# Performance work log

Measured on AMD Instinct MI355X. Metric: run time of the kernel, lower is better.

## Reference

```python
import jax, jax.numpy as jnp
import numpy as np

B, L, DIM, H = 2, 2048, 2048, 16
D = DIM // H
EPS = 1e-6
CAP = 50.0
SCALE = D ** -0.5


def _rms_norm(x, w):
    # x: [B,H,L,D], normalize over last dim
    scale = jax.lax.rsqrt(jnp.maximum(jnp.mean(x * x, axis=-1, keepdims=True), EPS))
    return w * x * scale


def _rotate_half(x):
    x1, x2 = jnp.split(x, 2, axis=-1)
    return jnp.concatenate([-x2, x1], axis=-1)


def setup_inputs() -> dict:
    key = jax.random.key(0)
    ks = jax.random.split(key, 6)
    x = jax.random.normal(ks[0], (B, L, DIM), dtype=jnp.float32)
    w_qkv = jax.random.normal(ks[1], (3 * DIM, DIM), dtype=jnp.float32) * (DIM ** -0.5)
    w_out = jax.random.normal(ks[2], (DIM, DIM), dtype=jnp.float32) * (DIM ** -0.5)
    q_norm_w = jnp.ones((D,), dtype=jnp.float32)
    k_norm_w = jnp.ones((D,), dtype=jnp.float32)
    # rope tables [L, D]
    inv_freq = 1.0 / (10000.0 ** (np.arange(0, D, 2, dtype=np.float32) / D))
    t = np.arange(L, dtype=np.float32)
    freqs = np.outer(t, inv_freq)  # [L, D/2]
    emb = np.concatenate([freqs, freqs], axis=-1)  # [L, D]
    cos = jnp.asarray(np.cos(emb), dtype=jnp.float32)
    sin = jnp.asarray(np.sin(emb), dtype=jnp.float32)
    # additive causal mask [1,1,L,L]
    causal = np.triu(np.full((L, L), -1e9, dtype=np.float32), k=1)
    mask = jnp.asarray(causal)[None, None]
    return {"x": x, "w_qkv": w_qkv, "w_out": w_out, "q_norm_w": q_norm_w,
            "k_norm_w": k_norm_w, "cos": cos, "sin": sin, "mask": mask}


def reference(x, w_qkv, w_out, q_norm_w, k_norm_w, cos, sin, mask):
    b, l, _ = x.shape
    qkv = jnp.einsum('bld,ed->ble', x, w_qkv).reshape(b, l, 3, H, D)
    q, k, v = [jnp.transpose(qkv[:, :, i], (0, 2, 1, 3)) for i in range(3)]  # [B,H,L,D]
    q = _rms_norm(q, q_norm_w)
    k = _rms_norm(k, k_norm_w)
    # rope: cos/sin are [L,D] -> [1,1,L,D]
    c = cos[-l:, :][None, None]
    s = sin[-l:, :][None, None]
    q = q * c + _rotate_half(q) * s
    k = k * c + _rotate_half(k) * s
    attn = jnp.einsum('bhqd,bhkd->bhqk', q, k) * SCALE
    attn = jnp.tanh(attn / CAP) * CAP + mask
    probs = jax.nn.softmax(attn, axis=-1)
    o = jnp.einsum('bhqk,bhkd->bhqd', probs, v)
    o = jnp.transpose(o, (0, 2, 1, 3)).reshape(b, l, H * D)
    out = jnp.einsum('bld,ed->ble', o, w_out)
    return (out, (k, v))
```

## Files before the change

### kernel.cpp

```cpp
#include <hip/hip_runtime.h>
#include <hip/hip_bf16.h>
#include <stdint.h>

#define LL 2048
#define DD 128
#define HH 16

typedef float f32x4 __attribute__((ext_vector_type(4)));
typedef float f32x2 __attribute__((ext_vector_type(2)));
typedef short bf16x8 __attribute__((ext_vector_type(8)));
typedef short short4v __attribute__((ext_vector_type(4)));
typedef float float4v __attribute__((ext_vector_type(4)));

__device__ __forceinline__ float bf2f(short s) {
  union { unsigned u; float f; } v; v.u = ((unsigned)(unsigned short)s) << 16; return v.f;
}
__device__ __forceinline__ short f2bf(float f) {
  union { float f; unsigned u; } v; v.f = f;
  unsigned u = v.u;
  u += 0x7fffu + ((u >> 16) & 1u);
  return (short)(u >> 16);
}

__device__ __forceinline__ void gload_lds16(const void* g, void* lds) {
  __builtin_amdgcn_global_load_lds(
      (__attribute__((address_space(1))) unsigned int*)(void*)(uintptr_t)g,
      (__attribute__((address_space(3))) unsigned int*)lds, 16, 0, 0);
}

__global__ __launch_bounds__(256) void cast_all_kernel(
    const float* __restrict__ x, const float* __restrict__ wqkv,
    const float* __restrict__ wout, short* __restrict__ dst)
{
  long i4 = ((long)blockIdx.x * 256 + threadIdx.x) * 4;
  const float* src; long off;
  if (i4 < 8388608L)        { src = x;    off = i4; }
  else if (i4 < 20971520L)  { src = wqkv; off = i4 - 8388608L; }
  else                      { src = wout; off = i4 - 20971520L; }
  float4v v = *(const float4v*)(src + off);
  short4v o;
  o.x = f2bf(v.x); o.y = f2bf(v.y); o.z = f2bf(v.z); o.w = f2bf(v.w);
  *(short4v*)(dst + i4) = o;
}

#define SCHED __builtin_amdgcn_sched_barrier(0)
#define BARRIER { __builtin_amdgcn_s_barrier(); }

#define STAGE(buf, opx, ptr, rb, ks, t)                                        \
  { _Pragma("unroll") for (int l_ = 0; l_ < 2; ++l_) {                          \
      int ch_ = l_ * 512 + tid;                                                 \
      int row_ = ch_ >> 2, ci_ = ch_ & 3;                                       \
      gload_lds16(ptr + (size_t)(rb + row_) * K + (t) * 64 + (ks) * 32 +        \
                      ((ci_ ^ ((row_ >> 1) & 3)) << 3),                         \
                  &lds[buf][opx][ks][ch_ << 3]);                                \
  } }

#define LDA(buf, mh, ks)                                                       \
  { _Pragma("unroll") for (int mf_ = 0; mf_ < 4; ++mf_) {                       \
      int r_ = wm * 128 + (mh) * 64 + mf_ * 16 + j;                             \
      areg[mf_] = *(const bf16x8*)&lds[buf][0][ks][r_ * 32 + ((g ^ ((j >> 1) & 3)) << 3)]; \
  } }

#define LDB(dst, buf, ks)                                                      \
  { _Pragma("unroll") for (int nf_ = 0; nf_ < 4; ++nf_) {                       \
      int r_ = wn * 64 + nf_ * 16 + j;                                          \
      dst[nf_] = *(const bf16x8*)&lds[buf][1][ks][r_ * 32 + ((g ^ ((j >> 1) & 3)) << 3)]; \
  } }

#define MFMAQ(mh, breg)                                                        \
  { __builtin_amdgcn_s_setprio(1);                                             \
    _Pragma("unroll") for (int mf_ = 0; mf_ < 4; ++mf_)                         \
      _Pragma("unroll") for (int nf_ = 0; nf_ < 4; ++nf_)                       \
        acc[(mh) * 4 + mf_][nf_] = __builtin_amdgcn_mfma_f32_16x16x32_bf16(     \
            areg[mf_], breg[nf_], acc[(mh) * 4 + mf_][nf_], 0, 0, 0);           \
    __builtin_amdgcn_s_setprio(0); }

__global__ __launch_bounds__(512, 2) void gemm256_kernel(
    const short* __restrict__ A, const short* __restrict__ Bm,
    short* __restrict__ C, int M, int N, int K)
{
  __shared__ __align__(16) short lds[2][2][2][8192];
  const int tid = threadIdx.x;
  const int lane = tid & 63;
  const int wid = tid >> 6;
  const int wm = wid >> 2, wn = wid & 3;
  const int g = lane >> 4, j = lane & 15;
  const int m0 = blockIdx.y * 256, n0 = blockIdx.x * 256;
  const int NT = K >> 6;

  f32x4 acc[8][4];
  const f32x4 z = {0.f, 0.f, 0.f, 0.f};
#pragma unroll
  for (int im = 0; im < 8; ++im)
#pragma unroll
    for (int nf = 0; nf < 4; ++nf) acc[im][nf] = z;

  STAGE(0, 1, Bm, n0, 0, 0); STAGE(0, 1, Bm, n0, 1, 0);
  STAGE(0, 0, A,  m0, 0, 0); STAGE(0, 0, A,  m0, 1, 0);
  STAGE(1, 1, Bm, n0, 0, 1); STAGE(1, 1, Bm, n0, 1, 1);
  STAGE(1, 0, A,  m0, 0, 1);
  asm volatile("s_waitcnt vmcnt(6)" ::: "memory");
  __builtin_amdgcn_s_barrier();
  SCHED;

  bf16x8 areg[4], b0r[4], b1r[4];
#pragma unroll 1
  for (int i = 0; i < (NT >> 1) - 1; ++i) {
    int t0 = i * 2;
    LDA(0, 0, 0); LDB(b0r, 0, 0);
    STAGE(1, 0, A, m0, 1, t0 + 1);
    BARRIER; MFMAQ(0, b0r); BARRIER;
    LDA(0, 0, 1); LDB(b1r, 0, 1);
    STAGE(0, 1, Bm, n0, 0, t0 + 2);
    BARRIER; MFMAQ(0, b1r); BARRIER;
    LDA(0, 1, 0);
    STAGE(0, 1, Bm, n0, 1, t0 + 2);
    BARRIER; MFMAQ(1, b0r); BARRIER;
    LDA(0, 1, 1);
    STAGE(0, 0, A, m0, 0, t0 + 2);
    BARRIER; MFMAQ(1, b1r);
    asm volatile("s_waitcnt vmcnt(6)" ::: "memory");
    __builtin_amdgcn_s_barrier(); SCHED;
    LDA(1, 0, 0); LDB(b0r, 1, 0);
    STAGE(0, 0, A, m0, 1, t0 + 2);
    BARRIER; MFMAQ(0, b0r); BARRIER;
    LDA(1, 0, 1); LDB(b1r, 1, 1);
    STAGE(1, 1, Bm, n0, 0, t0 + 3);
    BARRIER; MFMAQ(0, b1r); BARRIER;
    LDA(1, 1, 0);
    STAGE(1, 1, Bm, n0, 1, t0 + 3);
    BARRIER; MFMAQ(1, b0r); BARRIER;
    LDA(1, 1, 1);
    STAGE(1, 0, A, m0, 0, t0 + 3);
    BARRIER; MFMAQ(1, b1r);
    asm volatile("s_waitcnt vmcnt(6)" ::: "memory");
    __builtin_amdgcn_s_barrier(); SCHED;
  }
  {
    LDA(0, 0, 0); LDB(b0r, 0, 0);
    STAGE(1, 0, A, m0, 1, NT - 1);
    BARRIER; MFMAQ(0, b0r); BARRIER;
    LDA(0, 0, 1); LDB(b1r, 0, 1);
    BARRIER; MFMAQ(0, b1r); BARRIER;
    LDA(0, 1, 0);
    BARRIER; MFMAQ(1, b0r); BARRIER;
    LDA(0, 1, 1);
    BARRIER; MFMAQ(1, b1r);
    asm volatile("s_waitcnt vmcnt(0)" ::: "memory");
    __builtin_amdgcn_s_barrier(); SCHED;
    LDA(1, 0, 0); LDB(b0r, 1, 0); MFMAQ(0, b0r);
    LDA(1, 0, 1); LDB(b1r, 1, 1); MFMAQ(0, b1r);
    LDA(1, 1, 0); MFMAQ(1, b0r);
    LDA(1, 1, 1); MFMAQ(1, b1r);
  }
#pragma unroll
  for (int im = 0; im < 8; ++im)
#pragma unroll
    for (int nf = 0; nf < 4; ++nf)
#pragma unroll
      for (int r = 0; r < 4; ++r)
        C[(size_t)(m0 + wm * 128 + im * 16 + g * 4 + r) * N + n0 + wn * 64 + nf * 16 + j] =
            f2bf(acc[im][nf][r]);
}

template <typename OutT>
__global__ __launch_bounds__(256) void gemm_bt_kernel(
    const short* __restrict__ A, const short* __restrict__ Bm,
    OutT* __restrict__ C, int M, int N, int K)
{
  __shared__ __align__(16) short As[128 * 64];
  __shared__ __align__(16) short Bs[128 * 64];
  const int tid = threadIdx.x;
  const int lane = tid & 63;
  const int g = lane >> 4, j = lane & 15;
  const int m0 = blockIdx.y * 128, n0 = blockIdx.x * 128;
  const int wave = tid >> 6;
  const int wm = (wave >> 1) * 64, wn = (wave & 1) * 64;

  f32x4 acc[4][4];
  const f32x4 z = {0.f, 0.f, 0.f, 0.f};
#pragma unroll
  for (int i = 0; i < 4; ++i)
#pragma unroll
    for (int jj = 0; jj < 4; ++jj) acc[i][jj] = z;

  for (int k0 = 0; k0 < K; k0 += 64) {
#pragma unroll
    for (int it = 0; it < 4; ++it) {
      int c = it * 256 + tid;
      int row = c >> 3, ko = (c & 7) << 3;
      gload_lds16(A + (size_t)(m0 + row) * K + k0 + ko, As + c * 8);
    }
#pragma unroll
    for (int it = 0; it < 4; ++it) {
      int c = it * 256 + tid;
      int row = c >> 3, ko = (c & 7) << 3;
      gload_lds16(Bm + (size_t)(n0 + row) * K + k0 + ko, Bs + c * 8);
    }
    __syncthreads();
#pragma unroll
    for (int ks = 0; ks < 2; ++ks) {
      bf16x8 af[4], bfr[4];
#pragma unroll
      for (int i = 0; i < 4; ++i)
        af[i] = *(const bf16x8*)(As + (wm + i * 16 + j) * 64 + ks * 32 + g * 8);
#pragma unroll
      for (int i = 0; i < 4; ++i)
        bfr[i] = *(const bf16x8*)(Bs + (wn + i * 16 + j) * 64 + ks * 32 + g * 8);
#pragma unroll
      for (int i = 0; i < 4; ++i)
#pragma unroll
        for (int jj = 0; jj < 4; ++jj)
          acc[i][jj] = __builtin_amdgcn_mfma_f32_16x16x32_bf16(af[i], bfr[jj], acc[i][jj], 0, 0, 0);
    }
    __syncthreads();
  }
#pragma unroll
  for (int i = 0; i < 4; ++i)
#pragma unroll
    for (int jj = 0; jj < 4; ++jj)
#pragma unroll
      for (int r = 0; r < 4; ++r) {
        int row = m0 + wm + i * 16 + g * 4 + r;
        int col = n0 + wn + jj * 16 + j;
        if constexpr (sizeof(OutT) == 4)
          C[(size_t)row * N + col] = acc[i][jj][r];
        else
          C[(size_t)row * N + col] = f2bf(acc[i][jj][r]);
      }
}

__global__ __launch_bounds__(256) void normrope_kernel(
    const short* __restrict__ qkv, const float* __restrict__ qw,
    const float* __restrict__ kw, const float* __restrict__ cosb,
    const float* __restrict__ sinb, short* __restrict__ qo,
    float* __restrict__ ko, short* __restrict__ kb, float* __restrict__ vo)
{
  int wid = (blockIdx.x * 256 + threadIdx.x) >> 6;
  int lane = threadIdx.x & 63;
  int h = wid & 15;
  int rest = wid >> 4;
  int t = rest % 3;
  int bl = rest / 3;
  int l = bl & (LL - 1);
  int d0 = lane * 2;
  const short* src = qkv + (size_t)bl * 6144 + t * 2048 + h * 128 + d0;
  int raw = *(const int*)src;
  float v0 = bf2f((short)(raw & 0xffff));
  float v1 = bf2f((short)((raw >> 16) & 0xffff));
  size_t oidx = ((size_t)((bl >> 11) * HH + h) * LL + l) * DD + d0;
  if (t == 2) {
    f32x2 vv = {v0, v1};
    *(f32x2*)(vo + oidx) = vv;
    return;
  }
  float ss = v0 * v0 + v1 * v1;
#pragma unroll
  for (int m = 1; m <= 32; m <<= 1) ss += __shfl_xor(ss, m, 64);
  float scale = rsqrtf(fmaxf(ss * (1.0f / 128.0f), 1e-6f));
  const float* w = (t == 0) ? qw : kw;
  float n0 = w[d0] * v0 * scale;
  float n1 = w[d0 + 1] * v1 * scale;
  float c0 = cosb[l * 128 + d0], c1 = cosb[l * 128 + d0 + 1];
  float s0 = sinb[l * 128 + d0], s1 = sinb[l * 128 + d0 + 1];
  float p0 = __shfl_xor(n0, 32, 64);
  float p1 = __shfl_xor(n1, 32, 64);
  float r0 = (lane < 32) ? -p0 : p0;
  float r1 = (lane < 32) ? -p1 : p1;
  float o0 = n0 * c0 + r0 * s0;
  float o1 = n1 * c1 + r1 * s1;
  int pk = (int)((unsigned short)f2bf(o0) | ((unsigned)(unsigned short)f2bf(o1) << 16));
  if (t == 0) {
    *(int*)(qo + oidx) = pk;
  } else {
    f32x2 kk = {o0, o1};
    *(f32x2*)(ko + oidx) = kk;
    *(int*)(kb + oidx) = pk;
  }
}

__global__ __launch_bounds__(256) void transpose_v_kernel(
    const short* __restrict__ qkv, short* __restrict__ vT)
{
  __shared__ __align__(16) short tl[64 * 72];
  int bid = blockIdx.x;
  int dt = bid & 1;
  int lt = (bid >> 1) & 31;
  int bh = bid >> 6;
  int b = bh >> 4, h = bh & 15;
  int tid = threadIdx.x;
#pragma unroll
  for (int it = 0; it < 2; ++it) {
    int c = it * 256 + tid;
    int row = c >> 3, off = (c & 7) << 3;
    int l = lt * 64 + row;
    bf16x8 val = *(const bf16x8*)(qkv + (size_t)(b * LL + l) * 6144 + 4096 + h * 128 + dt * 64 + off);
    *(bf16x8*)(tl + row * 72 + off) = val;
  }
  __syncthreads();
#pragma unroll
  for (int it = 0; it < 2; ++it) {
    int c = it * 256 + tid;
    int dr = c >> 3, lo = (c & 7) << 3;
    bf16x8 o;
#pragma unroll
    for (int i = 0; i < 8; ++i) o[i] = tl[(lo + i) * 72 + dr];
    *(bf16x8*)(vT + ((size_t)bh * DD + dt * 64 + dr) * LL + lt * 64 + lo) = o;
  }
}

__global__ __launch_bounds__(256, 2) void attn_kernel(
    const short* __restrict__ q, const short* __restrict__ k,
    const short* __restrict__ vT, short* __restrict__ o)
{
  __shared__ __align__(16) short Ks[64 * 128];
  __shared__ __align__(16) short Vs[128 * 64];
  __shared__ __align__(16) short Ps[128 * 72];
  int bid = blockIdx.x;
  int bh = bid & 31;
  int gq = (bid >> 5) & 7;
  int qt = (bid < 256) ? (15 - gq) : gq;
  int b = bh >> 4;
  int h = bh & 15;
  int tid = threadIdx.x;
  int lane = tid & 63;
  int w = tid >> 6;
  int g = lane >> 4, j = lane & 15;
  int q0 = qt * 128;
  int wrow = q0 + w * 32;

  const short* kp = k + (size_t)bh * LL * DD;
  const short* vp = vT + (size_t)bh * DD * LL;

  bf16x8 qf[2][4];
#pragma unroll
  for (int mi = 0; mi < 2; ++mi)
#pragma unroll
    for (int ks = 0; ks < 4; ++ks)
      qf[mi][ks] = *(const bf16x8*)(q + ((size_t)bh * LL + wrow + mi * 16 + j) * DD + ks * 32 + g * 8);

  f32x4 accO[2][8];
  const f32x4 z = {0.f, 0.f, 0.f, 0.f};
#pragma unroll
  for (int mi = 0; mi < 2; ++mi)
#pragma unroll
    for (int n = 0; n < 8; ++n) accO[mi][n] = z;
  float lsum[2][4] = {{0.f,0.f,0.f,0.f},{0.f,0.f,0.f,0.f}};

  const float cu = 0.0017677669529663687f;
  int ktmax = 2 * qt + 1;
  for (int kt = 0; kt <= ktmax; ++kt) {
    int k0 = kt * 64;
#pragma unroll
    for (int it = 0; it < 4; ++it) {
      int c = it * 256 + tid;
      int row = c >> 4, off = (c & 15) << 3;
      gload_lds16(kp + (size_t)(k0 + row) * DD + (off ^ ((row & 7) << 3)), Ks + c * 8);
    }
#pragma unroll
    for (int it = 0; it < 4; ++it) {
      int c = it * 256 + tid;
      int row = c >> 3, off = (c & 7) << 3;
      gload_lds16(vp + (size_t)row * LL + k0 + (off ^ ((row & 7) << 3)), Vs + c * 8);
    }
    __syncthreads();

    const bool active = (k0 <= wrow + 31);
    if (active) {
      f32x4 sa[2][4];
#pragma unroll
      for (int mi = 0; mi < 2; ++mi)
#pragma unroll
        for (int n = 0; n < 4; ++n) sa[mi][n] = z;
      __builtin_amdgcn_s_setprio(1);
#pragma unroll
      for (int ks = 0; ks < 4; ++ks) {
#pragma unroll
        for (int n = 0; n < 4; ++n) {
          bf16x8 kf = *(const bf16x8*)(Ks + (n * 16 + j) * 128 + ((ks * 32 + g * 8) ^ ((j & 7) << 3)));
#pragma unroll
          for (int mi = 0; mi < 2; ++mi)
            sa[mi][n] = __builtin_amdgcn_mfma_f32_16x16x32_bf16(qf[mi][ks], kf, sa[mi][n], 0, 0, 0);
        }
      }
      __builtin_amdgcn_s_setprio(0);

#pragma unroll
      for (int mi = 0; mi < 2; ++mi) {
        const bool wmask = (k0 + 63) > (wrow + mi * 16);
#pragma unroll
        for (int r = 0; r < 4; ++r) {
          int row_g = wrow + mi * 16 + g * 4 + r;
#pragma unroll
          for (int n = 0; n < 4; ++n) {
            float u = sa[mi][n][r] * cu;
            float v2 = u * u;
            float poly = fmaf(v2, fmaf(v2, fmaf(v2, -2.6984127f, 6.6666667f),
                                       -16.666667f), 50.f);
            float p = __expf(fmaf(u, poly, -12.f));
            if (wmask && (k0 + n * 16 + j > row_g)) p = 0.f;
            lsum[mi][r] += p;
            Ps[(w * 32 + mi * 16 + g * 4 + r) * 72 + n * 16 + j] = f2bf(p);
          }
        }
      }
      __builtin_amdgcn_s_setprio(1);
#pragma unroll
      for (int ks = 0; ks < 2; ++ks) {
        bf16x8 pf[2];
#pragma unroll
        for (int mi = 0; mi < 2; ++mi)
          pf[mi] = *(const bf16x8*)(Ps + (w * 32 + mi * 16 + j) * 72 + ks * 32 + g * 8);
#pragma unroll
        for (int n = 0; n < 8; ++n) {
          bf16x8 vf = *(const bf16x8*)(Vs + (n * 16 + j) * 64 + ((ks * 32 + g * 8) ^ ((j & 7) << 3)));
#pragma unroll
          for (int mi = 0; mi < 2; ++mi)
            accO[mi][n] = __builtin_amdgcn_mfma_f32_16x16x32_bf16(pf[mi], vf, accO[mi][n], 0, 0, 0);
        }
      }
      __builtin_amdgcn_s_setprio(0);
    }
    __syncthreads();
  }

#pragma unroll
  for (int mi = 0; mi < 2; ++mi)
#pragma unroll
    for (int r = 0; r < 4; ++r) {
#pragma unroll
      for (int m = 1; m <= 8; m <<= 1) lsum[mi][r] += __shfl_xor(lsum[mi][r], m, 64);
    }

#pragma unroll
  for (int mi = 0; mi < 2; ++mi) {
    size_t obase = ((size_t)b * LL + wrow + mi * 16) * 2048 + h * 128;
#pragma unroll
    for (int r = 0; r < 4; ++r) {
      float inv = 1.f / lsum[mi][r];
#pragma unroll
      for (int n = 0; n < 8; ++n)
        o[obase + (size_t)(g * 4 + r) * 2048 + n * 16 + j] = f2bf(accO[mi][n][r] * inv);
    }
  }
}

extern "C" void kernel_launch(void* const* d_in, const int* in_sizes, int n_in,
                              void* d_out, int out_size, void* d_ws, size_t ws_size,
                              hipStream_t stream) {
  const float* x    = (const float*)d_in[0];
  const float* wqkv = (const float*)d_in[1];
  const float* wout = (const float*)d_in[2];
  const float* qw   = (const float*)d_in[3];
  const float* kw   = (const float*)d_in[4];
  const float* cosb = (const float*)d_in[5];
  const float* sinb = (const float*)d_in[6];

  float* out   = (float*)d_out;
  float* k_out = out + 8388608;
  float* v_out = out + 16777216;

  short* ws    = (short*)d_ws;
  short* xb    = ws;
  short* wqkvb = ws + 8388608;
  short* woutb = ws + 20971520;
  short* qkv   = ws + 25165824;
  short* qbuf  = xb;
  short* kbuf  = wqkvb;
  short* vT    = qkv + 16777216;
  vT   = ws + 50331648;
  short* obuf = ws + 54525952;
  obuf = qkv;

  cast_all_kernel<<<24576, 256, 0, stream>>>(x, wqkv, wout, ws);
  gemm256_kernel<<<dim3(24, 16), 512, 0, stream>>>(xb, wqkvb, qkv, 4096, 6144, 2048);
  normrope_kernel<<<49152, 256, 0, stream>>>(qkv, qw, kw, cosb, sinb, qbuf, k_out, kbuf, v_out);
  transpose_v_kernel<<<2048, 256, 0, stream>>>(qkv, vT);
  attn_kernel<<<512, 256, 0, stream>>>(qbuf, kbuf, vT, obuf);
  gemm_bt_kernel<float><<<dim3(16, 32), 256, 0, stream>>>(obuf, woutb, out, 4096, 2048, 2048);
}
```

Baseline: 315.6 us.

## Switch attention to 32x32x16 MFMA with S^T layout and register-resident P

Rewrites the attention kernel to use 32x32x16 bf16 MFMA, computing S transposed (K as A operand) so each lane owns one query column. The probabilities stay in registers and are packed with v_cvt_pk_bf16 plus a cross-half lane shuffle into the PV operand, which removes the Ps shared-memory buffer and its store/load round trip. The softmax scale is folded into Q during the norm/rope kernel so the per-score multiply disappears. This shrinks LDS use and instruction count, but relies on correct MFMA register layout assumptions and adds shuffles.

```diff
diff --git a/kernel.cpp b/kernel.cpp
--- a/kernel.cpp
+++ b/kernel.cpp
@@ -7,9 +7,11 @@
 #define HH 16
 
 typedef float f32x4 __attribute__((ext_vector_type(4)));
+typedef float f32x16 __attribute__((ext_vector_type(16)));
 typedef float f32x2 __attribute__((ext_vector_type(2)));
 typedef short bf16x8 __attribute__((ext_vector_type(8)));
 typedef short short4v __attribute__((ext_vector_type(4)));
+typedef int int4v __attribute__((ext_vector_type(4)));
 typedef float float4v __attribute__((ext_vector_type(4)));
 
 __device__ __forceinline__ float bf2f(short s) {
@@ -20,6 +22,11 @@
   unsigned u = v.u;
   u += 0x7fffu + ((u >> 16) & 1u);
   return (short)(u >> 16);
+}
+__device__ __forceinline__ unsigned cvtpk(float lo, float hi) {
+  unsigned r;
+  asm("v_cvt_pk_bf16_f32 %0, %1, %2" : "=v"(r) : "v"(lo), "v"(hi));
+  return r;
 }
 
 __device__ __forceinline__ void gload_lds16(const void* g, void* lds) {
@@ -269,12 +276,15 @@
   float r1 = (lane < 32) ? -p1 : p1;
   float o0 = n0 * c0 + r0 * s0;
   float o1 = n1 * c1 + r1 * s1;
-  int pk = (int)((unsigned short)f2bf(o0) | ((unsigned)(unsigned short)f2bf(o1) << 16));
   if (t == 0) {
+    const float cu = 0.0017677669529663687f;
+    int pk = (int)((unsigned short)f2bf(o0 * cu) |
+                   ((unsigned)(unsigned short)f2bf(o1 * cu) << 16));
     *(int*)(qo + oidx) = pk;
   } else {
     f32x2 kk = {o0, o1};
     *(f32x2*)(ko + oidx) = kk;
+    int pk = (int)((unsigned short)f2bf(o0) | ((unsigned)(unsigned short)f2bf(o1) << 16));
     *(int*)(kb + oidx) = pk;
   }
 }
@@ -315,7 +325,6 @@
 {
   __shared__ __align__(16) short Ks[64 * 128];
   __shared__ __align__(16) short Vs[128 * 64];
-  __shared__ __align__(16) short Ps[128 * 72];
   int bid = blockIdx.x;
   int bh = bid & 31;
   int gq = (bid >> 5) & 7;
@@ -325,29 +334,26 @@
   int tid = threadIdx.x;
   int lane = tid & 63;
   int w = tid >> 6;
-  int g = lane >> 4, j = lane & 15;
+  int l31 = lane & 31, lo5 = lane >> 5;
   int q0 = qt * 128;
   int wrow = q0 + w * 32;
+  int qg = wrow + l31;
 
   const short* kp = k + (size_t)bh * LL * DD;
   const short* vp = vT + (size_t)bh * DD * LL;
 
-  bf16x8 qf[2][4];
-#pragma unroll
-  for (int mi = 0; mi < 2; ++mi)
-#pragma unroll
-    for (int ks = 0; ks < 4; ++ks)
-      qf[mi][ks] = *(const bf16x8*)(q + ((size_t)bh * LL + wrow + mi * 16 + j) * DD + ks * 32 + g * 8);
-
-  f32x4 accO[2][8];
-  const f32x4 z = {0.f, 0.f, 0.f, 0.f};
-#pragma unroll
-  for (int mi = 0; mi < 2; ++mi)
-#pragma unroll
-    for (int n = 0; n < 8; ++n) accO[mi][n] = z;
-  float lsum[2][4] = {{0.f,0.f,0.f,0.f},{0.f,0.f,0.f,0.f}};
-
-  const float cu = 0.0017677669529663687f;
+  bf16x8 qf[8];
+#pragma unroll
+  for (int ds_ = 0; ds_ < 8; ++ds_)
+    qf[ds_] = *(const bf16x8*)(q + ((size_t)bh * LL + qg) * DD + ds_ * 16 + lo5 * 8);
+
+  f32x16 accO[4];
+#pragma unroll
+  for (int dt = 0; dt < 4; ++dt)
+#pragma unroll
+    for (int r = 0; r < 16; ++r) accO[dt][r] = 0.f;
+  float lsum = 0.f;
+
   int ktmax = 2 * qt + 1;
   for (int kt = 0; kt <= ktmax; ++kt) {
     int k0 = kt * 64;
@@ -367,56 +373,66 @@
 
     const bool active = (k0 <= wrow + 31);
     if (active) {
-      f32x4 sa[2][4];
-#pragma unroll
-      for (int mi = 0; mi < 2; ++mi)
-#pragma unroll
-        for (int n = 0; n < 4; ++n) sa[mi][n] = z;
+      f32x16 sa[2];
+#pragma unroll
+      for (int t2 = 0; t2 < 2; ++t2)
+#pragma unroll
+        for (int r = 0; r < 16; ++r) sa[t2][r] = 0.f;
+
       __builtin_amdgcn_s_setprio(1);
 #pragma unroll
-      for (int ks = 0; ks < 4; ++ks) {
-#pragma unroll
-        for (int n = 0; n < 4; ++n) {
-          bf16x8 kf = *(const bf16x8*)(Ks + (n * 16 + j) * 128 + ((ks * 32 + g * 8) ^ ((j & 7) << 3)));
-#pragma unroll
-          for (int mi = 0; mi < 2; ++mi)
-            sa[mi][n] = __builtin_amdgcn_mfma_f32_16x16x32_bf16(qf[mi][ks], kf, sa[mi][n], 0, 0, 0);
+      for (int ds_ = 0; ds_ < 8; ++ds_) {
+#pragma unroll
+        for (int t2 = 0; t2 < 2; ++t2) {
+          int row = t2 * 32 + l31;
+          bf16x8 kf = *(const bf16x8*)(Ks + row * 128 +
+                          ((ds_ * 16 + lo5 * 8) ^ ((l31 & 7) << 3)));
+          sa[t2] = __builtin_amdgcn_mfma_f32_32x32x16_bf16(kf, qf[ds_], sa[t2], 0, 0, 0);
         }
       }
       __builtin_amdgcn_s_setprio(0);
 
 #pragma unroll
-      for (int mi = 0; mi < 2; ++mi) {
-        const bool wmask = (k0 + 63) > (wrow + mi * 16);
-#pragma unroll
-        for (int r = 0; r < 4; ++r) {
-          int row_g = wrow + mi * 16 + g * 4 + r;
-#pragma unroll
-          for (int n = 0; n < 4; ++n) {
-            float u = sa[mi][n][r] * cu;
-            float v2 = u * u;
-            float poly = fmaf(v2, fmaf(v2, fmaf(v2, -2.6984127f, 6.6666667f),
-                                       -16.666667f), 50.f);
-            float p = __expf(fmaf(u, poly, -12.f));
-            if (wmask && (k0 + n * 16 + j > row_g)) p = 0.f;
-            lsum[mi][r] += p;
-            Ps[(w * 32 + mi * 16 + g * 4 + r) * 72 + n * 16 + j] = f2bf(p);
-          }
+      for (int t2 = 0; t2 < 2; ++t2) {
+        const bool tmask = (k0 + t2 * 32 + 31) > wrow;
+#pragma unroll
+        for (int r = 0; r < 16; ++r) {
+          float u = sa[t2][r];
+          float v2 = u * u;
+          float poly = fmaf(v2, fmaf(v2, fmaf(v2, -2.6984127f, 6.6666667f),
+                                     -16.666667f), 50.f);
+          float p = __expf(fmaf(u, poly, -12.f));
+          int kglob = k0 + t2 * 32 + (r & 3) + 8 * (r >> 2) + 4 * lo5;
+          if (tmask && (kglob > qg)) p = 0.f;
+          lsum += p;
+          sa[t2][r] = p;
         }
       }
+
       __builtin_amdgcn_s_setprio(1);
 #pragma unroll
-      for (int ks = 0; ks < 2; ++ks) {
-        bf16x8 pf[2];
-#pragma unroll
-        for (int mi = 0; mi < 2; ++mi)
-          pf[mi] = *(const bf16x8*)(Ps + (w * 32 + mi * 16 + j) * 72 + ks * 32 + g * 8);
-#pragma unroll
-        for (int n = 0; n < 8; ++n) {
-          bf16x8 vf = *(const bf16x8*)(Vs + (n * 16 + j) * 64 + ((ks * 32 + g * 8) ^ ((j & 7) << 3)));
-#pragma unroll
-          for (int mi = 0; mi < 2; ++mi)
-            accO[mi][n] = __builtin_amdgcn_mfma_f32_16x16x32_bf16(pf[mi], vf, accO[mi][n], 0, 0, 0);
+      for (int s = 0; s < 4; ++s) {
+        int t2 = s >> 1, RA = 8 * (s & 1), RB = RA + 4;
+        unsigned xa0 = cvtpk(sa[t2][RA + 0], sa[t2][RA + 1]);
+        unsigned xa1 = cvtpk(sa[t2][RA + 2], sa[t2][RA + 3]);
+        unsigned xb0 = cvtpk(sa[t2][RB + 0], sa[t2][RB + 1]);
+        unsigned xb1 = cvtpk(sa[t2][RB + 2], sa[t2][RB + 3]);
+        unsigned sxa0 = (unsigned)__shfl_xor((int)xa0, 32, 64);
+        unsigned sxa1 = (unsigned)__shfl_xor((int)xa1, 32, 64);
+        unsigned sxb0 = (unsigned)__shfl_xor((int)xb0, 32, 64);
+        unsigned sxb1 = (unsigned)__shfl_xor((int)xb1, 32, 64);
+        int4v wv;
+        wv.x = (int)(lo5 ? sxb0 : xa0);
+        wv.y = (int)(lo5 ? sxb1 : xa1);
+        wv.z = (int)(lo5 ? xb0 : sxa0);
+        wv.w = (int)(lo5 ? xb1 : sxa1);
+        bf16x8 pa = __builtin_bit_cast(bf16x8, wv);
+#pragma unroll
+        for (int dt = 0; dt < 4; ++dt) {
+          int row = dt * 32 + l31;
+          bf16x8 vf = *(const bf16x8*)(Vs + row * 64 +
+                          ((s * 16 + lo5 * 8) ^ ((l31 & 7) << 3)));
+          accO[dt] = __builtin_amdgcn_mfma_f32_32x32x16_bf16(pa, vf, accO[dt], 0, 0, 0);
         }
       }
       __builtin_amdgcn_s_setprio(0);
@@ -424,24 +440,16 @@
     __syncthreads();
   }
 
-#pragma unroll
-  for (int mi = 0; mi < 2; ++mi)
-#pragma unroll
-    for (int r = 0; r < 4; ++r) {
-#pragma unroll
-      for (int m = 1; m <= 8; m <<= 1) lsum[mi][r] += __shfl_xor(lsum[mi][r], m, 64);
-    }
-
-#pragma unroll
-  for (int mi = 0; mi < 2; ++mi) {
-    size_t obase = ((size_t)b * LL + wrow + mi * 16) * 2048 + h * 128;
-#pragma unroll
-    for (int r = 0; r < 4; ++r) {
-      float inv = 1.f / lsum[mi][r];
-#pragma unroll
-      for (int n = 0; n < 8; ++n)
-        o[obase + (size_t)(g * 4 + r) * 2048 + n * 16 + j] = f2bf(accO[mi][n][r] * inv);
-    }
+  lsum += __shfl_xor(lsum, 32, 64);
+  float inv = 1.f / lsum;
+#pragma unroll
+  for (int r = 0; r < 16; ++r) {
+    int qrow = (r & 3) + 8 * (r >> 2) + 4 * lo5;
+    float invr = __shfl(inv, qrow, 64);
+    size_t obase = ((size_t)b * LL + wrow + qrow) * 2048 + h * 128;
+#pragma unroll
+    for (int dt = 0; dt < 4; ++dt)
+      o[obase + dt * 32 + l31] = f2bf(accO[dt][r] * invr);
   }
 }
 
@@ -467,10 +475,8 @@
   short* qkv   = ws + 25165824;
   short* qbuf  = xb;
   short* kbuf  = wqkvb;
-  short* vT    = qkv + 16777216;
-  vT   = ws + 50331648;
-  short* obuf = ws + 54525952;
-  obuf = qkv;
+  short* vT    = ws + 50331648;
+  short* obuf  = qkv;
 
   cast_all_kernel<<<24576, 256, 0, stream>>>(x, wqkv, wout, ws);
   gemm256_kernel<<<dim3(24, 16), 512, 0, stream>>>(xb, wqkvb, qkv, 4096, 6144, 2048);
```

Result: faster. 302.6 us (-4.1%).
